# Kernel tuning notes

Hardware: AMD Instinct MI355X
Metric: run time of the kernel (lower is better)

The kernel has to match this reference:

```python
import jax, jax.numpy as jnp
import numpy as np

OFFS = [(0, 0), (1, 0), (-1, 0), (0, 1), (0, -1), (1, -1), (-1, 1)]  # (dq, dr)
B, H, W, E, NH, L = 16, 64, 64, 254, 8, 8
C = E + 2          # d_model = 256
DFF = 4 * C        # 1024
MLP = 512
VOCAB = 9


def setup_inputs():
    ks = jax.random.split(jax.random.key(0), 24)
    r = lambda k, s: jax.random.normal(k, s, dtype=jnp.float32) * 0.05
    return {
        'grid': jax.random.randint(ks[0], (B, H, W), 0, VOCAB),
        'gold': jax.random.normal(ks[1], (B, 2), dtype=jnp.float32),
        'emb': r(ks[2], (VOCAB, E)),
        'in_w': r(ks[3], (L, 3 * C, C)), 'in_b': r(ks[4], (L, 3 * C)),
        'out_w': r(ks[5], (L, C, C)), 'out_b': r(ks[6], (L, C)),
        'l1_w': r(ks[7], (L, DFF, C)), 'l1_b': r(ks[8], (L, DFF)),
        'l2_w': r(ks[9], (L, C, DFF)), 'l2_b': r(ks[10], (L, C)),
        'n1_g': jnp.ones((L, C)), 'n1_b': jnp.zeros((L, C)),
        'n2_g': jnp.ones((L, C)), 'n2_b': jnp.zeros((L, C)),
        'fn_g': jnp.ones((C,)), 'fn_b': jnp.zeros((C,)),
        'pw1': r(ks[11], (MLP, C)), 'pb1': r(ks[12], (MLP,)),
        'pw2': r(ks[13], (3, MLP)), 'pb2': r(ks[14], (3,)),
        'cw1': r(ks[15], (128, C)), 'cb1': r(ks[16], (128,)),
        'cw2': r(ks[17], (1, 128)), 'cb2': r(ks[18], (1,)),
    }


def _ln(x, g, b, eps=1e-5):
    m = jnp.mean(x, -1, keepdims=True)
    v = jnp.mean(jnp.square(x - m), -1, keepdims=True)
    return (x - m) * jax.lax.rsqrt(v + eps) * g + b


def _hex_gather(x):
    # x: (B,H,W,C) -> (B,H,W,7,C); out-of-bounds neighbors are zero vectors
    b, h, w, c = x.shape
    xp = jnp.pad(x, ((0, 0), (1, 1), (1, 1), (0, 0)))
    feats = [xp[:, 1 + dr:1 + dr + h, 1 + dq:1 + dq + w, :] for (dq, dr) in OFFS]
    return jnp.stack(feats, axis=3)


def _mha(x, kv, w_in, b_in, w_out, b_out):
    # x: (B,H,W,C) queries; kv: (B,H,W,7,C); full-bias projections, no mask
    c = x.shape[-1]
    hd = c // NH
    wq, wk, wv = w_in[:c], w_in[c:2 * c], w_in[2 * c:]
    bq, bk, bv = b_in[:c], b_in[c:2 * c], b_in[2 * c:]
    q = (x @ wq.T + bq).reshape(*x.shape[:-1], NH, hd)
    k = (kv @ wk.T + bk).reshape(*kv.shape[:-1], NH, hd)
    v = (kv @ wv.T + bv).reshape(*kv.shape[:-1], NH, hd)
    scores = jnp.einsum('bxyne,bxykne->bxynk', q, k) / np.sqrt(hd).astype(np.float32)
    attn = jax.nn.softmax(scores, axis=-1)
    o = jnp.einsum('bxynk,bxykne->bxyne', attn, v)
    o = o.reshape(*x.shape[:-1], c)
    return o @ w_out.T + b_out


def _pos_embed(h, w, d):
    half = d // 2
    div = jnp.exp(jnp.arange(0, half, 2, dtype=jnp.float32) * (-np.log(10000.0) / half))
    pw = jnp.arange(w, dtype=jnp.float32)[:, None] * div
    pe_w = jnp.concatenate([jnp.sin(pw), jnp.cos(pw)], -1)  # (W, 2*len(div))
    ph = jnp.arange(h, dtype=jnp.float32)[:, None] * div
    pe_h = jnp.concatenate([jnp.sin(ph), jnp.cos(ph)], -1)
    cw, ch = pe_w.shape[-1], pe_h.shape[-1]
    pe = jnp.zeros((h, w, d), dtype=jnp.float32)
    pe = pe.at[:, :, :cw].set(jnp.broadcast_to(pe_w[None, :, :], (h, w, cw)))
    pe = pe.at[:, :, cw:cw + ch].set(jnp.broadcast_to(pe_h[:, None, :], (h, w, ch)))
    return pe


def _forward(grid, gold, emb, in_w, in_b, out_w, out_b, l1_w, l1_b, l2_w, l2_b,
             n1_g, n1_b, n2_g, n2_b, fn_g, fn_b, pw1, pb1, pw2, pb2, cw1, cb1, cw2, cb2):
    b, h, w = grid.shape
    feats = jnp.concatenate(
        [emb[grid], jnp.broadcast_to(gold[:, None, None, :], (b, h, w, 2))], -1)
    x = feats + _pos_embed(h, w, C)[None]
    for i in range(L):
        kvg = _hex_gather(x)
        a = _mha(x, kvg, in_w[i], in_b[i], out_w[i], out_b[i])
        x = _ln(x + a, n1_g[i], n1_b[i])
        ff = jax.nn.relu(x @ l1_w[i].T + l1_b[i]) @ l2_w[i].T + l2_b[i]
        x = _ln(x + ff, n2_g[i], n2_b[i])
    x = _ln(x, fn_g, fn_b)
    pooled = jnp.mean(x, axis=(1, 2))  # (B,C) critic adaptive-avg-pool
    value = (jax.nn.relu(pooled @ cw1.T + cb1) @ cw2.T + cb2)[:, 0]
    pol = jax.nn.relu(x @ pw1.T + pb1) @ pw2.T + pb2  # (B,H,W,3)
    return pol[..., 2], pol[..., 0], pol[..., 1], value


def reference(grid, gold, emb, in_w, in_b, out_w, out_b, l1_w, l1_b, l2_w, l2_b,
              n1_g, n1_b, n2_g, n2_b, fn_g, fn_b, pw1, pb1, pw2, pb2, cw1, cb1, cw2, cb2):
    return _forward(grid, gold, emb, in_w, in_b, out_w, out_b, l1_w, l1_b, l2_w, l2_b,
                    n1_g, n1_b, n2_g, n2_b, fn_g, fn_b, pw1, pb1, pw2, pb2,
                    cw1, cb1, cw2, cb2)
```

## Files before the change

### kernel.cpp

```cpp
#include <hip/hip_runtime.h>

typedef __bf16 bf16x8 __attribute__((ext_vector_type(8)));
typedef float  f32x4  __attribute__((ext_vector_type(4)));
typedef unsigned short u16;
typedef u16 u16x8 __attribute__((ext_vector_type(8)));
typedef u16 u16x4 __attribute__((ext_vector_type(4)));

__device__ __forceinline__ float bf2f(u16 h) {
  union { unsigned u; float f; } w; w.u = ((unsigned)h) << 16; return w.f;
}
__device__ __forceinline__ u16 f2bf(float f) {
  union { float f; unsigned u; } w; w.f = f;
  return (u16)((w.u + 0x7fffu + ((w.u >> 16) & 1u)) >> 16);
}

__global__ __launch_bounds__(256)
void cvt_kernel(const float* __restrict__ src, u16* __restrict__ dst, int n) {
  int i = blockIdx.x * 256 + threadIdx.x;
  if (i < n) dst[i] = f2bf(src[i]);
}

__global__ __launch_bounds__(256)
void embed_kernel(const int* __restrict__ grd, const float* __restrict__ gold,
                  const float* __restrict__ emb, u16* __restrict__ xbf) {
  int t = blockIdx.x, c = threadIdx.x;
  int b = t >> 12, y = (t >> 6) & 63, xw = t & 63;
  int g = grd[t];
  float v = (c < 254) ? emb[g * 254 + c] : gold[b * 2 + (c - 254)];
  int j = c & 63;
  float dv = expf(-(float)(2 * j) * (9.210340371976184f / 128.0f));
  float arg = ((c < 128) ? (float)xw : (float)y) * dv;
  v += (c & 64) ? cosf(arg) : sinf(arg);
  xbf[(long)t * 256 + c] = f2bf(v);
}

template<int RELU, int ROWS>
__global__ __launch_bounds__(256)
void gemm_qn(const u16* __restrict__ A, const u16* __restrict__ W,
             const float* __restrict__ bias, u16* __restrict__ out,
             int Nout, int NT) {
  constexpr int NI = ROWS / 32;
  __shared__ u16 sA[ROWS * 256];
  __shared__ u16 sW[128 * 64];
  int tid = threadIdx.x;
  int lane = tid & 63, wave = tid >> 6;
  int wr = wave >> 1, wc = wave & 1;
  long rowbase = (long)blockIdx.x * ROWS;
  unsigned lbase = (unsigned)(tid & ~63) * 16;

  {
    int ac = tid & 31;
#pragma unroll
    for (int p = 0; p < ROWS / 8; ++p) {
      int row = p * 8 + (tid >> 5);
      int sc = (ac & 24) | ((ac ^ row) & 7);
      const u16* src = A + (rowbase + row) * 256 + sc * 8;
      __builtin_amdgcn_global_load_lds(
          (const __attribute__((address_space(1))) void*)src,
          (__attribute__((address_space(3))) void*)((char*)sA + p * 4096 + lbase),
          16, 0, 0);
    }
  }

  f32x4 acc[NI][4] = {};
  int T = NT * 4;
  for (int t = 0; t < T; ++t) {
    int nt = t >> 2, kc = t & 3;
    __syncthreads();
#pragma unroll
    for (int p = 0; p < 4; ++p) {
      int row = p * 32 + (tid >> 3);
      int sc = ((tid & 7) ^ row) & 7;
      const u16* src = W + (long)(nt * 128 + row) * 256 + kc * 64 + sc * 8;
      __builtin_amdgcn_global_load_lds(
          (const __attribute__((address_space(1))) void*)src,
          (__attribute__((address_space(3))) void*)((char*)sW + p * 4096 + lbase),
          16, 0, 0);
    }
    __syncthreads();

#pragma unroll
    for (int kk = 0; kk < 2; ++kk) {
      bf16x8 af[NI], bw[4];
#pragma unroll
      for (int i = 0; i < NI; ++i) {
        int ra = wr * (ROWS / 2) + i * 16 + (lane & 15);
        int l = kc * 8 + kk * 4 + (lane >> 4);
        int phys = (l & 24) | ((l ^ ra) & 7);
        af[i] = *(const bf16x8*)((const char*)sA + ra * 512 + phys * 16);
      }
#pragma unroll
      for (int j = 0; j < 4; ++j) {
        int rb = wc * 64 + j * 16 + (lane & 15);
        int m = kk * 4 + (lane >> 4);
        int phys = (m ^ rb) & 7;
        bw[j] = *(const bf16x8*)((const char*)sW + rb * 128 + phys * 16);
      }
#pragma unroll
      for (int i = 0; i < NI; ++i)
#pragma unroll
        for (int j = 0; j < 4; ++j)
          acc[i][j] = __builtin_amdgcn_mfma_f32_16x16x32_bf16(af[i], bw[j], acc[i][j], 0, 0, 0);
    }

    if (kc == 3) {
#pragma unroll
      for (int i = 0; i < NI; ++i) {
        long r0 = rowbase + wr * (ROWS / 2) + i * 16 + ((lane >> 4) * 4);
#pragma unroll
        for (int j = 0; j < 4; ++j) {
          long col = (long)nt * 128 + wc * 64 + j * 16 + (lane & 15);
          float bv = bias[col];
#pragma unroll
          for (int r = 0; r < 4; ++r) {
            float v = acc[i][j][r] + bv;
            if (RELU) v = fmaxf(v, 0.0f);
            out[(r0 + r) * Nout + col] = f2bf(v);
            acc[i][j][r] = 0.0f;
          }
        }
      }
    }
  }
}

__global__ __launch_bounds__(256)
void gemm_pol(const u16* __restrict__ A, const u16* __restrict__ W,
              const float* __restrict__ b1, const float* __restrict__ pw2,
              const float* __restrict__ pb2, float* __restrict__ out) {
  __shared__ u16 sA[64 * 256];
  __shared__ u16 sW[128 * 64];
  __shared__ float part[2][3][64];
  int tid = threadIdx.x;
  int lane = tid & 63, wave = tid >> 6;
  int wr = wave >> 1, wc = wave & 1;
  long rowbase = (long)blockIdx.x * 64;
  unsigned lbase = (unsigned)(tid & ~63) * 16;

  for (int i = tid; i < 384; i += 256) ((float*)part)[i] = 0.0f;

  {
    int ac = tid & 31;
#pragma unroll
    for (int p = 0; p < 8; ++p) {
      int row = p * 8 + (tid >> 5);
      int sc = (ac & 24) | ((ac ^ row) & 7);
      const u16* src = A + (rowbase + row) * 256 + sc * 8;
      __builtin_amdgcn_global_load_lds(
          (const __attribute__((address_space(1))) void*)src,
          (__attribute__((address_space(3))) void*)((char*)sA + p * 4096 + lbase),
          16, 0, 0);
    }
  }

  f32x4 acc[2][4] = {};
  for (int t = 0; t < 16; ++t) {
    int nt = t >> 2, kc = t & 3;
    __syncthreads();
#pragma unroll
    for (int p = 0; p < 4; ++p) {
      int row = p * 32 + (tid >> 3);
      int sc = ((tid & 7) ^ row) & 7;
      const u16* src = W + (long)(nt * 128 + row) * 256 + kc * 64 + sc * 8;
      __builtin_amdgcn_global_load_lds(
          (const __attribute__((address_space(1))) void*)src,
          (__attribute__((address_space(3))) void*)((char*)sW + p * 4096 + lbase),
          16, 0, 0);
    }
    __syncthreads();

#pragma unroll
    for (int kk = 0; kk < 2; ++kk) {
      bf16x8 af[2], bw[4];
#pragma unroll
      for (int i = 0; i < 2; ++i) {
        int ra = wr * 32 + i * 16 + (lane & 15);
        int l = kc * 8 + kk * 4 + (lane >> 4);
        int phys = (l & 24) | ((l ^ ra) & 7);
        af[i] = *(const bf16x8*)((const char*)sA + ra * 512 + phys * 16);
      }
#pragma unroll
      for (int j = 0; j < 4; ++j) {
        int rb = wc * 64 + j * 16 + (lane & 15);
        int m = kk * 4 + (lane >> 4);
        int phys = (m ^ rb) & 7;
        bw[j] = *(const bf16x8*)((const char*)sW + rb * 128 + phys * 16);
      }
#pragma unroll
      for (int i = 0; i < 2; ++i)
#pragma unroll
        for (int j = 0; j < 4; ++j)
          acc[i][j] = __builtin_amdgcn_mfma_f32_16x16x32_bf16(af[i], bw[j], acc[i][j], 0, 0, 0);
    }

    if (kc == 3) {
#pragma unroll
      for (int i = 0; i < 2; ++i) {
#pragma unroll
        for (int r = 0; r < 4; ++r) {
          float p0 = 0.f, p1 = 0.f, p2 = 0.f;
#pragma unroll
          for (int j = 0; j < 4; ++j) {
            int col = nt * 128 + wc * 64 + j * 16 + (lane & 15);
            float v = fmaxf(acc[i][j][r] + b1[col], 0.0f);
            p0 += v * pw2[col];
            p1 += v * pw2[512 + col];
            p2 += v * pw2[1024 + col];
            acc[i][j][r] = 0.0f;
          }
#pragma unroll
          for (int m = 1; m < 16; m <<= 1) {
            p0 += __shfl_xor(p0, m); p1 += __shfl_xor(p1, m); p2 += __shfl_xor(p2, m);
          }
          if ((lane & 15) == 0) {
            int row = wr * 32 + i * 16 + (lane >> 4) * 4 + r;
            part[wc][0][row] += p0;
            part[wc][1][row] += p1;
            part[wc][2][row] += p2;
          }
        }
      }
    }
  }

  __syncthreads();
  if (tid < 64) {
    long t = rowbase + tid;
    float a0 = part[0][0][tid] + part[1][0][tid];
    float a1 = part[0][1][tid] + part[1][1][tid];
    float a2 = part[0][2][tid] + part[1][2][tid];
    out[t]          = a2 + pb2[2];
    out[65536 + t]  = a0 + pb2[0];
    out[131072 + t] = a1 + pb2[1];
  }
}

template<int KC>
__global__ __launch_bounds__(256)
void gemm_rln(const u16* __restrict__ A, int lda, const u16* __restrict__ W,
              const float* __restrict__ bias, u16* __restrict__ xbf,
              const float* __restrict__ g, const float* __restrict__ b) {
  __shared__ __align__(16) char smem[40960];
  u16* sAr = (u16*)smem;
  u16* sWr = (u16*)(smem + 8192);
  float* red = (float*)smem;
  int tid = threadIdx.x;
  int lane = tid & 63, wave = tid >> 6;
  long rowbase = (long)blockIdx.x * 64;
  unsigned lbase = (unsigned)(tid & ~63) * 16;

  f32x4 acc[4][4] = {};
  for (int kc = 0; kc < KC; ++kc) {
    __syncthreads();
#pragma unroll
    for (int p = 0; p < 2; ++p) {
      int row = p * 32 + (tid >> 3);
      int sc = ((tid & 7) ^ row) & 7;
      const u16* src = A + (rowbase + row) * lda + kc * 64 + sc * 8;
      __builtin_amdgcn_global_load_lds(
          (const __attribute__((address_space(1))) void*)src,
          (__attribute__((address_space(3))) void*)((char*)sAr + p * 4096 + lbase),
          16, 0, 0);
    }
#pragma unroll
    for (int p = 0; p < 8; ++p) {
      int row = p * 32 + (tid >> 3);
      int sc = ((tid & 7) ^ row) & 7;
      const u16* src = W + (long)row * (KC * 64) + kc * 64 + sc * 8;
      __builtin_amdgcn_global_load_lds(
          (const __attribute__((address_space(1))) void*)src,
          (__attribute__((address_space(3))) void*)((char*)sWr + p * 4096 + lbase),
          16, 0, 0);
    }
    __syncthreads();

#pragma unroll
    for (int kk = 0; kk < 2; ++kk) {
      bf16x8 af[4], bw[4];
#pragma unroll
      for (int i = 0; i < 4; ++i) {
        int ra = i * 16 + (lane & 15);
        int m = kk * 4 + (lane >> 4);
        int phys = (m ^ ra) & 7;
        af[i] = *(const bf16x8*)((const char*)sAr + ra * 128 + phys * 16);
      }
#pragma unroll
      for (int j = 0; j < 4; ++j) {
        int rb = wave * 64 + j * 16 + (lane & 15);
        int m = kk * 4 + (lane >> 4);
        int phys = (m ^ rb) & 7;
        bw[j] = *(const bf16x8*)((const char*)sWr + rb * 128 + phys * 16);
      }
#pragma unroll
      for (int i = 0; i < 4; ++i)
#pragma unroll
        for (int j = 0; j < 4; ++j)
          acc[i][j] = __builtin_amdgcn_mfma_f32_16x16x32_bf16(af[i], bw[j], acc[i][j], 0, 0, 0);
    }
  }

  float gcol[4], bcol[4];
  long colb = wave * 64 + (lane & 15);
#pragma unroll
  for (int j = 0; j < 4; ++j) { gcol[j] = g[colb + j * 16]; bcol[j] = b[colb + j * 16]; }

  __syncthreads();

#pragma unroll
  for (int i = 0; i < 4; ++i) {
#pragma unroll
    for (int r = 0; r < 4; ++r) {
      int rowl = i * 16 + (lane >> 4) * 4 + r;
      long rbase = (rowbase + rowl) * 256;
      float ps = 0.f, pss = 0.f;
#pragma unroll
      for (int j = 0; j < 4; ++j) {
        float v = acc[i][j][r] + bias[colb + j * 16] + bf2f(xbf[rbase + colb + j * 16]);
        acc[i][j][r] = v;
        ps += v; pss += v * v;
      }
#pragma unroll
      for (int m = 1; m < 16; m <<= 1) { ps += __shfl_xor(ps, m); pss += __shfl_xor(pss, m); }
      if ((lane & 15) == 0) {
        red[wave * 64 + rowl] = ps;
        red[256 + wave * 64 + rowl] = pss;
      }
    }
  }
  __syncthreads();
  if (tid < 64) {
    float s = red[tid] + red[64 + tid] + red[128 + tid] + red[192 + tid];
    float ss = red[256 + tid] + red[320 + tid] + red[384 + tid] + red[448 + tid];
    float mean = s * (1.0f / 256.0f);
    float var = ss * (1.0f / 256.0f) - mean * mean;
    red[512 + tid * 2] = mean;
    red[512 + tid * 2 + 1] = rsqrtf(var + 1e-5f);
  }
  __syncthreads();

#pragma unroll
  for (int i = 0; i < 4; ++i) {
#pragma unroll
    for (int r = 0; r < 4; ++r) {
      int rowl = i * 16 + (lane >> 4) * 4 + r;
      float mean = red[512 + rowl * 2];
      float rstd = red[512 + rowl * 2 + 1];
      long rbase = (rowbase + rowl) * 256;
#pragma unroll
      for (int j = 0; j < 4; ++j) {
        float o = (acc[i][j][r] - mean) * rstd * gcol[j] + bcol[j];
        xbf[rbase + colb + j * 16] = f2bf(o);
      }
    }
  }
}

__global__ __launch_bounds__(256)
void attn_kernel(u16* __restrict__ qkv, const float* __restrict__ bin) {
  const int drA[7] = {0, 0, 0, 1, -1, -1, 1};
  const int dqA[7] = {0, 1, -1, 0, 0, 1, -1};
  int bid = blockIdx.x;
  int bswz = (bid & 7) * 512 + (bid >> 3);
  int gid = bswz * 256 + threadIdx.x;
  int t = gid >> 4;
  int sub = gid & 15;
  int hoff = sub * 16;
  int b = t >> 12, y = (t >> 6) & 63, xw = t & 63;
  long tbase = (long)t * 768 + hoff;

  long tn[7]; float okf[7];
#pragma unroll
  for (int n = 0; n < 7; ++n) {
    int yy = y + drA[n], xx = xw + dqA[n];
    bool ok = ((unsigned)yy < 64u) && ((unsigned)xx < 64u);
    int yc = yy < 0 ? 0 : (yy > 63 ? 63 : yy);
    int xc = xx < 0 ? 0 : (xx > 63 ? 63 : xx);
    tn[n] = ((long)(b * 4096 + yc * 64 + xc)) * 768 + hoff;
    okf[n] = ok ? 1.0f : 0.0f;
  }

  u16x8 qraw[2], kr[7][2];
  {
    const u16x8* qp = (const u16x8*)(qkv + tbase);
    qraw[0] = qp[0]; qraw[1] = qp[1];
  }
#pragma unroll
  for (int n = 0; n < 7; ++n) {
    const u16x8* kp = (const u16x8*)(qkv + tn[n] + 256);
    kr[n][0] = kp[0]; kr[n][1] = kp[1];
  }

  float q[16];
#pragma unroll
  for (int j = 0; j < 2; ++j)
#pragma unroll
    for (int e = 0; e < 8; ++e) q[j * 8 + e] = bf2f(qraw[j][e]);

  float skb = 0.f;
  {
    const float* kb = bin + 256 + hoff;
#pragma unroll
    for (int i = 0; i < 16; ++i) skb += q[i] * kb[i];
  }

  float s[7];
#pragma unroll
  for (int n = 0; n < 7; ++n) {
    float acc = 0.f;
#pragma unroll
    for (int j = 0; j < 2; ++j)
#pragma unroll
      for (int e = 0; e < 8; ++e) acc += q[j * 8 + e] * bf2f(kr[n][j][e]);
    float p = (okf[n] != 0.f) ? acc : skb;
    p += __shfl_xor(p, 1);
    s[n] = p * 0.17677669529663687f;
  }

  u16x8 vr[7][2];
#pragma unroll
  for (int n = 0; n < 7; ++n) {
    const u16x8* vp = (const u16x8*)(qkv + tn[n] + 512);
    vr[n][0] = vp[0]; vr[n][1] = vp[1];
  }

  float mx = s[0];
#pragma unroll
  for (int n = 1; n < 7; ++n) mx = fmaxf(mx, s[n]);
  float wsum = 0.0f;
#pragma unroll
  for (int n = 0; n < 7; ++n) { s[n] = expf(s[n] - mx); wsum += s[n]; }
  float inv = 1.0f / wsum;

  float o[16];
#pragma unroll
  for (int i = 0; i < 16; ++i) o[i] = 0.0f;
  float woob = 0.f;
#pragma unroll
  for (int n = 0; n < 7; ++n) {
    float wk = okf[n] * s[n];
    woob += s[n] - wk;
#pragma unroll
    for (int j = 0; j < 2; ++j)
#pragma unroll
      for (int e = 0; e < 8; ++e) o[j * 8 + e] += wk * bf2f(vr[n][j][e]);
  }
  {
    const float* vb = bin + 512 + hoff;
#pragma unroll
    for (int i = 0; i < 16; ++i) o[i] += woob * vb[i];
  }

  u16x8* op = (u16x8*)(qkv + tbase);
#pragma unroll
  for (int j = 0; j < 2; ++j) {
    u16x8 ov;
#pragma unroll
    for (int e = 0; e < 8; ++e) ov[e] = f2bf(o[j * 8 + e] * inv);
    op[j] = ov;
  }
}

__global__ __launch_bounds__(256)
void ln_kernel(u16* __restrict__ xbf, const float* __restrict__ g,
               const float* __restrict__ b) {
  int wave = threadIdx.x >> 6, lane = threadIdx.x & 63;
  long t = (long)blockIdx.x * 4 + wave;
  long base = t * 256 + lane * 4;
  u16x4 raw = *(const u16x4*)(xbf + base);
  float v0 = bf2f(raw[0]), v1 = bf2f(raw[1]), v2 = bf2f(raw[2]), v3 = bf2f(raw[3]);
  float s = v0 + v1 + v2 + v3;
  float ss = v0 * v0 + v1 * v1 + v2 * v2 + v3 * v3;
#pragma unroll
  for (int m = 1; m < 64; m <<= 1) { s += __shfl_xor(s, m); ss += __shfl_xor(ss, m); }
  float mean = s * (1.0f / 256.0f);
  float var = ss * (1.0f / 256.0f) - mean * mean;
  float rstd = rsqrtf(var + 1e-5f);
  float4 gv = *(const float4*)(g + lane * 4);
  float4 bv = *(const float4*)(b + lane * 4);
  u16x4 ob;
  ob[0] = f2bf((v0 - mean) * rstd * gv.x + bv.x);
  ob[1] = f2bf((v1 - mean) * rstd * gv.y + bv.y);
  ob[2] = f2bf((v2 - mean) * rstd * gv.z + bv.z);
  ob[3] = f2bf((v3 - mean) * rstd * gv.w + bv.w);
  *(u16x4*)(xbf + base) = ob;
}

__global__ __launch_bounds__(256)
void pool1_kernel(const u16* __restrict__ xbf, float* __restrict__ part) {
  int bid = blockIdx.x, c = threadIdx.x;
  long base = (long)bid * 128 * 256;
  float s = 0.f;
  for (int p = 0; p < 128; ++p) s += bf2f(xbf[base + (long)p * 256 + c]);
  part[(long)bid * 256 + c] = s;
}
__global__ __launch_bounds__(256)
void pool2_kernel(const float* __restrict__ part, float* __restrict__ pooled) {
  int b = blockIdx.x, c = threadIdx.x;
  float s = 0.f;
  for (int seg = 0; seg < 32; ++seg) s += part[((long)b * 32 + seg) * 256 + c];
  pooled[b * 256 + c] = s * (1.0f / 4096.0f);
}

__global__ __launch_bounds__(128)
void value_kernel(const float* __restrict__ pooled, const float* __restrict__ cw1,
                  const float* __restrict__ cb1, const float* __restrict__ cw2,
                  const float* __restrict__ cb2, float* __restrict__ out) {
  int b = blockIdx.x, j = threadIdx.x;
  __shared__ float red[2];
  float hj = cb1[j];
  const float* pr = pooled + b * 256;
  const float* wr = cw1 + j * 256;
  for (int c = 0; c < 256; ++c) hj += pr[c] * wr[c];
  hj = fmaxf(hj, 0.0f);
  float acc = hj * cw2[j];
#pragma unroll
  for (int m = 1; m < 64; m <<= 1) acc += __shfl_xor(acc, m);
  if ((j & 63) == 0) red[j >> 6] = acc;
  __syncthreads();
  if (j == 0) out[196608 + b] = red[0] + red[1] + cb2[0];
}

extern "C" void kernel_launch(void* const* d_in, const int* in_sizes, int n_in,
                              void* d_out, int out_size, void* d_ws, size_t ws_size,
                              hipStream_t stream) {
  const int*   grd  = (const int*)d_in[0];
  const float* gold = (const float*)d_in[1];
  const float* emb  = (const float*)d_in[2];
  const float* in_w = (const float*)d_in[3];
  const float* in_b = (const float*)d_in[4];
  const float* out_w= (const float*)d_in[5];
  const float* out_b= (const float*)d_in[6];
  const float* l1_w = (const float*)d_in[7];
  const float* l1_b = (const float*)d_in[8];
  const float* l2_w = (const float*)d_in[9];
  const float* l2_b = (const float*)d_in[10];
  const float* n1_g = (const float*)d_in[11];
  const float* n1_b = (const float*)d_in[12];
  const float* n2_g = (const float*)d_in[13];
  const float* n2_b = (const float*)d_in[14];
  const float* fn_g = (const float*)d_in[15];
  const float* fn_b = (const float*)d_in[16];
  const float* pw1  = (const float*)d_in[17];
  const float* pb1  = (const float*)d_in[18];
  const float* pw2  = (const float*)d_in[19];
  const float* pb2  = (const float*)d_in[20];
  const float* cw1  = (const float*)d_in[21];
  const float* cb1  = (const float*)d_in[22];
  const float* cw2  = (const float*)d_in[23];
  const float* cb2  = (const float*)d_in[24];
  float* out = (float*)d_out;

  char* ws = (char*)d_ws;
  u16*   xbf    = (u16*)ws;
  char*  region = ws + (32l << 20);
  u16*   qkv    = (u16*)region;
  u16*   hbuf   = (u16*)region;
  u16*   wbf    = (u16*)(ws + (160l << 20));
  float* part   = (float*)(ws + (173l << 20));
  float* pooled = (float*)(ws + (174l << 20));

  u16* inw_bf  = wbf;
  u16* outw_bf = inw_bf + 1572864;
  u16* l1w_bf  = outw_bf + 524288;
  u16* l2w_bf  = l1w_bf + 2097152;
  u16* pw1_bf  = l2w_bf + 2097152;

  cvt_kernel<<<(1572864 + 255) / 256, 256, 0, stream>>>(in_w, inw_bf, 1572864);
  cvt_kernel<<<(524288 + 255) / 256, 256, 0, stream>>>(out_w, outw_bf, 524288);
  cvt_kernel<<<(2097152 + 255) / 256, 256, 0, stream>>>(l1_w, l1w_bf, 2097152);
  cvt_kernel<<<(2097152 + 255) / 256, 256, 0, stream>>>(l2_w, l2w_bf, 2097152);
  cvt_kernel<<<(131072 + 255) / 256, 256, 0, stream>>>(pw1, pw1_bf, 131072);

  embed_kernel<<<65536, 256, 0, stream>>>(grd, gold, emb, xbf);

  for (int i = 0; i < 8; ++i) {
    gemm_qn<0, 128><<<512, 256, 0, stream>>>(
        xbf, inw_bf + (long)i * 196608, in_b + i * 768, qkv, 768, 6);
    attn_kernel<<<4096, 256, 0, stream>>>(qkv, in_b + i * 768);
    gemm_rln<4><<<1024, 256, 0, stream>>>(
        qkv, 768, outw_bf + (long)i * 65536, out_b + i * 256, xbf,
        n1_g + i * 256, n1_b + i * 256);
    gemm_qn<1, 128><<<512, 256, 0, stream>>>(
        xbf, l1w_bf + (long)i * 262144, l1_b + i * 1024, hbuf, 1024, 8);
    gemm_rln<16><<<1024, 256, 0, stream>>>(
        hbuf, 1024, l2w_bf + (long)i * 262144, l2_b + i * 256, xbf,
        n2_g + i * 256, n2_b + i * 256);
  }

  ln_kernel<<<16384, 256, 0, stream>>>(xbf, fn_g, fn_b);

  gemm_pol<<<1024, 256, 0, stream>>>(xbf, pw1_bf, pb1, pw2, pb2, out);

  pool1_kernel<<<512, 256, 0, stream>>>(xbf, part);
  pool2_kernel<<<16, 256, 0, stream>>>(part, pooled);
  value_kernel<<<16, 128, 0, stream>>>(pooled, cw1, cb1, cw2, cb2, out);
}
```

Measured before the change: 1.923 ms.

## Load GEMM weight fragments directly from global memory, dropping LDS staging

The three GEMM kernels stop staging weight tiles (and in gemm_rln also the A tiles) through shared memory with per-step barriers. Each wave now loads its MFMA operand fragments straight from global memory, relying on cache for reuse across waves and blocks. This removes the LDS traffic and most of the __syncthreads calls in the K loop. In exchange it adds redundant global/L2 loads of the same weight rows by several waves, and load latency is no longer hidden by explicit staging.

```diff
diff --git a/kernel.cpp b/kernel.cpp
--- a/kernel.cpp
+++ b/kernel.cpp
@@ -41,10 +41,10 @@
              int Nout, int NT) {
   constexpr int NI = ROWS / 32;
   __shared__ u16 sA[ROWS * 256];
-  __shared__ u16 sW[128 * 64];
   int tid = threadIdx.x;
   int lane = tid & 63, wave = tid >> 6;
   int wr = wave >> 1, wc = wave & 1;
+  int g = lane >> 4;
   long rowbase = (long)blockIdx.x * ROWS;
   unsigned lbase = (unsigned)(tid & ~63) * 16;
 
@@ -61,40 +61,24 @@
           16, 0, 0);
     }
   }
-
-  f32x4 acc[NI][4] = {};
-  int T = NT * 4;
-  for (int t = 0; t < T; ++t) {
-    int nt = t >> 2, kc = t & 3;
-    __syncthreads();
-#pragma unroll
-    for (int p = 0; p < 4; ++p) {
-      int row = p * 32 + (tid >> 3);
-      int sc = ((tid & 7) ^ row) & 7;
-      const u16* src = W + (long)(nt * 128 + row) * 256 + kc * 64 + sc * 8;
-      __builtin_amdgcn_global_load_lds(
-          (const __attribute__((address_space(1))) void*)src,
-          (__attribute__((address_space(3))) void*)((char*)sW + p * 4096 + lbase),
-          16, 0, 0);
-    }
-    __syncthreads();
-
-#pragma unroll
-    for (int kk = 0; kk < 2; ++kk) {
+  __syncthreads();
+
+  for (int nt = 0; nt < NT; ++nt) {
+    f32x4 acc[NI][4] = {};
+#pragma unroll 2
+    for (int ks = 0; ks < 8; ++ks) {
       bf16x8 af[NI], bw[4];
+      int l = ks * 4 + g;
 #pragma unroll
       for (int i = 0; i < NI; ++i) {
         int ra = wr * (ROWS / 2) + i * 16 + (lane & 15);
-        int l = kc * 8 + kk * 4 + (lane >> 4);
         int phys = (l & 24) | ((l ^ ra) & 7);
         af[i] = *(const bf16x8*)((const char*)sA + ra * 512 + phys * 16);
       }
 #pragma unroll
       for (int j = 0; j < 4; ++j) {
-        int rb = wc * 64 + j * 16 + (lane & 15);
-        int m = kk * 4 + (lane >> 4);
-        int phys = (m ^ rb) & 7;
-        bw[j] = *(const bf16x8*)((const char*)sW + rb * 128 + phys * 16);
+        long rb = (long)nt * 128 + wc * 64 + j * 16 + (lane & 15);
+        bw[j] = *(const bf16x8*)(W + rb * 256 + ks * 32 + g * 8);
       }
 #pragma unroll
       for (int i = 0; i < NI; ++i)
@@ -102,22 +86,18 @@
         for (int j = 0; j < 4; ++j)
           acc[i][j] = __builtin_amdgcn_mfma_f32_16x16x32_bf16(af[i], bw[j], acc[i][j], 0, 0, 0);
     }
-
-    if (kc == 3) {
-#pragma unroll
-      for (int i = 0; i < NI; ++i) {
-        long r0 = rowbase + wr * (ROWS / 2) + i * 16 + ((lane >> 4) * 4);
-#pragma unroll
-        for (int j = 0; j < 4; ++j) {
-          long col = (long)nt * 128 + wc * 64 + j * 16 + (lane & 15);
-          float bv = bias[col];
-#pragma unroll
-          for (int r = 0; r < 4; ++r) {
-            float v = acc[i][j][r] + bv;
-            if (RELU) v = fmaxf(v, 0.0f);
-            out[(r0 + r) * Nout + col] = f2bf(v);
-            acc[i][j][r] = 0.0f;
-          }
+#pragma unroll
+    for (int i = 0; i < NI; ++i) {
+      long r0 = rowbase + wr * (ROWS / 2) + i * 16 + ((lane >> 4) * 4);
+#pragma unroll
+      for (int j = 0; j < 4; ++j) {
+        long col = (long)nt * 128 + wc * 64 + j * 16 + (lane & 15);
+        float bv = bias[col];
+#pragma unroll
+        for (int r = 0; r < 4; ++r) {
+          float v = acc[i][j][r] + bv;
+          if (RELU) v = fmaxf(v, 0.0f);
+          out[(r0 + r) * Nout + col] = f2bf(v);
         }
       }
     }
@@ -129,11 +109,11 @@
               const float* __restrict__ b1, const float* __restrict__ pw2,
               const float* __restrict__ pb2, float* __restrict__ out) {
   __shared__ u16 sA[64 * 256];
-  __shared__ u16 sW[128 * 64];
   __shared__ float part[2][3][64];
   int tid = threadIdx.x;
   int lane = tid & 63, wave = tid >> 6;
   int wr = wave >> 1, wc = wave & 1;
+  int g = lane >> 4;
   long rowbase = (long)blockIdx.x * 64;
   unsigned lbase = (unsigned)(tid & ~63) * 16;
 
@@ -152,39 +132,24 @@
           16, 0, 0);
     }
   }
-
-  f32x4 acc[2][4] = {};
-  for (int t = 0; t < 16; ++t) {
-    int nt = t >> 2, kc = t & 3;
-    __syncthreads();
-#pragma unroll
-    for (int p = 0; p < 4; ++p) {
-      int row = p * 32 + (tid >> 3);
-      int sc = ((tid & 7) ^ row) & 7;
-      const u16* src = W + (long)(nt * 128 + row) * 256 + kc * 64 + sc * 8;
-      __builtin_amdgcn_global_load_lds(
-          (const __attribute__((address_space(1))) void*)src,
-          (__attribute__((address_space(3))) void*)((char*)sW + p * 4096 + lbase),
-          16, 0, 0);
-    }
-    __syncthreads();
-
-#pragma unroll
-    for (int kk = 0; kk < 2; ++kk) {
+  __syncthreads();
+
+  for (int nt = 0; nt < 4; ++nt) {
+    f32x4 acc[2][4] = {};
+#pragma unroll 2
+    for (int ks = 0; ks < 8; ++ks) {
       bf16x8 af[2], bw[4];
+      int l = ks * 4 + g;
 #pragma unroll
       for (int i = 0; i < 2; ++i) {
         int ra = wr * 32 + i * 16 + (lane & 15);
-        int l = kc * 8 + kk * 4 + (lane >> 4);
         int phys = (l & 24) | ((l ^ ra) & 7);
         af[i] = *(const bf16x8*)((const char*)sA + ra * 512 + phys * 16);
       }
 #pragma unroll
       for (int j = 0; j < 4; ++j) {
-        int rb = wc * 64 + j * 16 + (lane & 15);
-        int m = kk * 4 + (lane >> 4);
-        int phys = (m ^ rb) & 7;
-        bw[j] = *(const bf16x8*)((const char*)sW + rb * 128 + phys * 16);
+        long rb = (long)nt * 128 + wc * 64 + j * 16 + (lane & 15);
+        bw[j] = *(const bf16x8*)(W + rb * 256 + ks * 32 + g * 8);
       }
 #pragma unroll
       for (int i = 0; i < 2; ++i)
@@ -192,32 +157,28 @@
         for (int j = 0; j < 4; ++j)
           acc[i][j] = __builtin_amdgcn_mfma_f32_16x16x32_bf16(af[i], bw[j], acc[i][j], 0, 0, 0);
     }
-
-    if (kc == 3) {
-#pragma unroll
-      for (int i = 0; i < 2; ++i) {
-#pragma unroll
-        for (int r = 0; r < 4; ++r) {
-          float p0 = 0.f, p1 = 0.f, p2 = 0.f;
-#pragma unroll
-          for (int j = 0; j < 4; ++j) {
-            int col = nt * 128 + wc * 64 + j * 16 + (lane & 15);
-            float v = fmaxf(acc[i][j][r] + b1[col], 0.0f);
-            p0 += v * pw2[col];
-            p1 += v * pw2[512 + col];
-            p2 += v * pw2[1024 + col];
-            acc[i][j][r] = 0.0f;
-          }
-#pragma unroll
-          for (int m = 1; m < 16; m <<= 1) {
-            p0 += __shfl_xor(p0, m); p1 += __shfl_xor(p1, m); p2 += __shfl_xor(p2, m);
-          }
-          if ((lane & 15) == 0) {
-            int row = wr * 32 + i * 16 + (lane >> 4) * 4 + r;
-            part[wc][0][row] += p0;
-            part[wc][1][row] += p1;
-            part[wc][2][row] += p2;
-          }
+#pragma unroll
+    for (int i = 0; i < 2; ++i) {
+#pragma unroll
+      for (int r = 0; r < 4; ++r) {
+        float p0 = 0.f, p1 = 0.f, p2 = 0.f;
+#pragma unroll
+        for (int j = 0; j < 4; ++j) {
+          int col = nt * 128 + wc * 64 + j * 16 + (lane & 15);
+          float v = fmaxf(acc[i][j][r] + b1[col], 0.0f);
+          p0 += v * pw2[col];
+          p1 += v * pw2[512 + col];
+          p2 += v * pw2[1024 + col];
+        }
+#pragma unroll
+        for (int m = 1; m < 16; m <<= 1) {
+          p0 += __shfl_xor(p0, m); p1 += __shfl_xor(p1, m); p2 += __shfl_xor(p2, m);
+        }
+        if ((lane & 15) == 0) {
+          int row = wr * 32 + i * 16 + (lane >> 4) * 4 + r;
+          part[wc][0][row] += p0;
+          part[wc][1][row] += p1;
+          part[wc][2][row] += p2;
         }
       }
     }
@@ -240,71 +201,37 @@
 void gemm_rln(const u16* __restrict__ A, int lda, const u16* __restrict__ W,
               const float* __restrict__ bias, u16* __restrict__ xbf,
               const float* __restrict__ g, const float* __restrict__ b) {
-  __shared__ __align__(16) char smem[40960];
-  u16* sAr = (u16*)smem;
-  u16* sWr = (u16*)(smem + 8192);
-  float* red = (float*)smem;
+  __shared__ float red[640];
   int tid = threadIdx.x;
   int lane = tid & 63, wave = tid >> 6;
+  int kg = lane >> 4;
   long rowbase = (long)blockIdx.x * 64;
-  unsigned lbase = (unsigned)(tid & ~63) * 16;
 
   f32x4 acc[4][4] = {};
-  for (int kc = 0; kc < KC; ++kc) {
-    __syncthreads();
-#pragma unroll
-    for (int p = 0; p < 2; ++p) {
-      int row = p * 32 + (tid >> 3);
-      int sc = ((tid & 7) ^ row) & 7;
-      const u16* src = A + (rowbase + row) * lda + kc * 64 + sc * 8;
-      __builtin_amdgcn_global_load_lds(
-          (const __attribute__((address_space(1))) void*)src,
-          (__attribute__((address_space(3))) void*)((char*)sAr + p * 4096 + lbase),
-          16, 0, 0);
-    }
-#pragma unroll
-    for (int p = 0; p < 8; ++p) {
-      int row = p * 32 + (tid >> 3);
-      int sc = ((tid & 7) ^ row) & 7;
-      const u16* src = W + (long)row * (KC * 64) + kc * 64 + sc * 8;
-      __builtin_amdgcn_global_load_lds(
-          (const __attribute__((address_space(1))) void*)src,
-          (__attribute__((address_space(3))) void*)((char*)sWr + p * 4096 + lbase),
-          16, 0, 0);
-    }
-    __syncthreads();
-
-#pragma unroll
-    for (int kk = 0; kk < 2; ++kk) {
-      bf16x8 af[4], bw[4];
-#pragma unroll
-      for (int i = 0; i < 4; ++i) {
-        int ra = i * 16 + (lane & 15);
-        int m = kk * 4 + (lane >> 4);
-        int phys = (m ^ ra) & 7;
-        af[i] = *(const bf16x8*)((const char*)sAr + ra * 128 + phys * 16);
-      }
-#pragma unroll
-      for (int j = 0; j < 4; ++j) {
-        int rb = wave * 64 + j * 16 + (lane & 15);
-        int m = kk * 4 + (lane >> 4);
-        int phys = (m ^ rb) & 7;
-        bw[j] = *(const bf16x8*)((const char*)sWr + rb * 128 + phys * 16);
-      }
-#pragma unroll
-      for (int i = 0; i < 4; ++i)
-#pragma unroll
-        for (int j = 0; j < 4; ++j)
-          acc[i][j] = __builtin_amdgcn_mfma_f32_16x16x32_bf16(af[i], bw[j], acc[i][j], 0, 0, 0);
-    }
+#pragma unroll 2
+  for (int ks = 0; ks < KC * 2; ++ks) {
+    bf16x8 af[4], bw[4];
+#pragma unroll
+    for (int i = 0; i < 4; ++i) {
+      long ra = rowbase + i * 16 + (lane & 15);
+      af[i] = *(const bf16x8*)(A + ra * lda + ks * 32 + kg * 8);
+    }
+#pragma unroll
+    for (int j = 0; j < 4; ++j) {
+      long rb = wave * 64 + j * 16 + (lane & 15);
+      bw[j] = *(const bf16x8*)(W + rb * (KC * 64) + ks * 32 + kg * 8);
+    }
+#pragma unroll
+    for (int i = 0; i < 4; ++i)
+#pragma unroll
+      for (int j = 0; j < 4; ++j)
+        acc[i][j] = __builtin_amdgcn_mfma_f32_16x16x32_bf16(af[i], bw[j], acc[i][j], 0, 0, 0);
   }
 
   float gcol[4], bcol[4];
   long colb = wave * 64 + (lane & 15);
 #pragma unroll
   for (int j = 0; j < 4; ++j) { gcol[j] = g[colb + j * 16]; bcol[j] = b[colb + j * 16]; }
-
-  __syncthreads();
 
 #pragma unroll
   for (int i = 0; i < 4; ++i) {
```

Result: slower. 2.952 ms (+53.5%).
